# Performance work log

Hardware: AMD Instinct MI355X
Metric: run time of the kernel (lower is better)

The kernel has to match this reference:

```python
import jax, jax.numpy as jnp
import numpy as np

HEADS = 8
LN_EPS = 1e-5

def setup_inputs() -> dict:
    key = jax.random.key(0)
    ks = jax.random.split(key, 12)
    B, T, N, D = 4, 24, 400, 256
    s = 1.0 / np.sqrt(D)
    x = jax.random.normal(ks[0], (B, T, N, D), dtype=jnp.float32)
    adj = jax.random.uniform(ks[1], (B, T, N, N), dtype=jnp.float32)
    Wq = jax.random.uniform(ks[2], (D, D), jnp.float32, -s, s)
    bq = jax.random.uniform(ks[3], (D,), jnp.float32, -s, s)
    Wk = jax.random.uniform(ks[4], (D, D), jnp.float32, -s, s)
    bk = jax.random.uniform(ks[5], (D,), jnp.float32, -s, s)
    Wv = jax.random.uniform(ks[6], (D, D), jnp.float32, -s, s)
    bv = jax.random.uniform(ks[7], (D,), jnp.float32, -s, s)
    gamma = jnp.ones((D,), jnp.float32)
    beta = jnp.zeros((D,), jnp.float32)
    return {"x": x, "adj": adj, "Wq": Wq, "bq": bq, "Wk": Wk, "bk": bk,
            "Wv": Wv, "bv": bv, "gamma": gamma, "beta": beta}

def reference(x, adj, Wq, bq, Wk, bk, Wv, bv, gamma, beta):
    B, T, N, D = x.shape
    H = HEADS
    hd = D // H
    # QKV projections (torch Linear: x @ W.T + b)
    q = (x @ Wq.T + bq).reshape(B, T, N, H, hd)
    k = (x @ Wk.T + bk).reshape(B, T, N, H, hd)
    v = (x @ Wv.T + bv).reshape(B, T, N, H, hd)
    # scores [B,T,H,N,N], scaled then multiplicatively masked by adj
    a = jnp.einsum('btnhd,btmhd->bthnm', q, k) / jnp.sqrt(jnp.float32(hd))
    a = a * adj[:, :, None, :, :]
    a = jax.nn.softmax(a, axis=-1)
    h = jnp.einsum('bthnm,btmhd->btnhd', a, v).reshape(B, T, N, D)
    # dropout is identity in eval; residual + LayerNorm
    y = h + x
    mu = jnp.mean(y, axis=-1, keepdims=True)
    var = jnp.mean((y - mu) ** 2, axis=-1, keepdims=True)
    return (y - mu) * jax.lax.rsqrt(var + LN_EPS) * gamma + beta
```

## Files before the change

### kernel.cpp

```cpp
#include <hip/hip_runtime.h>
#include <cstdint>
#include <cstddef>

typedef unsigned short u16;
typedef __attribute__((ext_vector_type(8))) __bf16 bf16x8;
typedef __attribute__((ext_vector_type(4))) float f32x4;
typedef __attribute__((ext_vector_type(8))) u16 u16x8;
typedef __attribute__((ext_vector_type(4))) u16 u16x4;

#define MTOT   38400
#define DMODEL 256
#define NQKV   768
#define NN     400
#define NBT    96
#define SCALE  0.17677669529663687f

__device__ __forceinline__ u16 f2b(float f){
  __bf16 b = (__bf16)f;
  return __builtin_bit_cast(u16, b);
}

__device__ __forceinline__ void g2l16(const void* g, void* l){
  __builtin_amdgcn_global_load_lds(
      (const __attribute__((address_space(1))) unsigned int*)g,
      (__attribute__((address_space(3))) unsigned int*)l,
      16, 0, 0);
}

__global__ __launch_bounds__(256) void cast_x_kernel(const float* __restrict__ x,
                                                     u16* __restrict__ xb, int n8){
  int i = blockIdx.x * 256 + threadIdx.x;
  if (i >= n8) return;
  const f32x4* xp = (const f32x4*)x;
  f32x4 a = xp[2*i], b = xp[2*i+1];
  u16x8 o;
  o[0]=f2b(a[0]); o[1]=f2b(a[1]); o[2]=f2b(a[2]); o[3]=f2b(a[3]);
  o[4]=f2b(b[0]); o[5]=f2b(b[1]); o[6]=f2b(b[2]); o[7]=f2b(b[3]);
  ((u16x8*)xb)[i] = o;
}

__global__ __launch_bounds__(256) void prep_w_kernel(
    const float* __restrict__ wq, const float* __restrict__ wk, const float* __restrict__ wv,
    const float* __restrict__ bq, const float* __restrict__ bk, const float* __restrict__ bv,
    u16* __restrict__ wqkv, float* __restrict__ bqkv){
  int i = blockIdx.x * 256 + threadIdx.x;
  int g = i >> 14;
  int rem = (i & 16383) * 4;
  const float* w = (g == 0) ? wq : ((g == 1) ? wk : wv);
  float sc = (g == 0) ? SCALE : 1.0f;
  f32x4 v = *(const f32x4*)(w + rem);
  u16x4 o; o[0]=f2b(v[0]*sc); o[1]=f2b(v[1]*sc); o[2]=f2b(v[2]*sc); o[3]=f2b(v[3]*sc);
  *(u16x4*)(wqkv + (size_t)i*4) = o;
  if (i < NQKV) bqkv[i] = (i < 256) ? bq[i]*SCALE : ((i < 512) ? bk[i-256] : bv[i-512]);
}

__global__ __launch_bounds__(256,2) void gemm_qkv_kernel(
    const u16* __restrict__ xb, const u16* __restrict__ wqkv,
    const float* __restrict__ bqkv, u16* __restrict__ qkv){
  __shared__ u16 a_lds[2][128*64];
  __shared__ u16 b_lds[2][128*64];
  const int tid = threadIdx.x, lane = tid & 63, wave = tid >> 6;
  const int bn = blockIdx.x % 6, bm = blockIdx.x / 6;
  const int m0 = bm*128, n0 = bn*128;
  const int wm = (wave>>1)*64, wn = (wave&1)*64;
  const int lr = lane & 15, lk = lane >> 4;
  f32x4 acc[4][4] = {};

  auto stage = [&](int buf, int k0){
    #pragma unroll
    for (int i = 0; i < 4; ++i){
      int off  = (wave*4 + i)*1024 + lane*16;
      int row  = off >> 7;
      int colb = off & 127;
      int scolb = colb ^ ((row & 7) << 4);
      g2l16(xb   + (size_t)(m0+row)*256 + k0 + (scolb>>1), (char*)a_lds[buf] + (wave*4+i)*1024);
      g2l16(wqkv + (size_t)(n0+row)*256 + k0 + (scolb>>1), (char*)b_lds[buf] + (wave*4+i)*1024);
    }
  };

  stage(0, 0);
  #pragma unroll
  for (int ks = 0; ks < 4; ++ks){
    if (ks < 3){
      stage((ks+1)&1, (ks+1)*64);
      asm volatile("s_waitcnt vmcnt(8)" ::: "memory");
    } else {
      asm volatile("s_waitcnt vmcnt(0)" ::: "memory");
    }
    __builtin_amdgcn_s_barrier();
    const char* al = (const char*)a_lds[ks&1];
    const char* bl = (const char*)b_lds[ks&1];
    #pragma unroll
    for (int sub = 0; sub < 2; ++sub){
      bf16x8 af[4], bfr[4];
      #pragma unroll
      for (int i = 0; i < 4; ++i){
        int ra = wm + i*16 + lr;
        af[i]  = *(const bf16x8*)(al + ra*128 + ((sub*64 + lk*16) ^ ((ra&7)<<4)));
        int rb = wn + i*16 + lr;
        bfr[i] = *(const bf16x8*)(bl + rb*128 + ((sub*64 + lk*16) ^ ((rb&7)<<4)));
      }
      #pragma unroll
      for (int i = 0; i < 4; ++i)
        #pragma unroll
        for (int j = 0; j < 4; ++j)
          acc[i][j] = __builtin_amdgcn_mfma_f32_16x16x32_bf16(af[i], bfr[j], acc[i][j], 0, 0, 0);
    }
    __builtin_amdgcn_s_barrier();
  }
  #pragma unroll
  for (int j = 0; j < 4; ++j){
    int n = n0 + wn + j*16 + lr;
    float bias = bqkv[n];
    #pragma unroll
    for (int i = 0; i < 4; ++i){
      int mb = m0 + wm + i*16 + lk*4;
      #pragma unroll
      for (int r = 0; r < 4; ++r)
        qkv[(size_t)(mb + r)*NQKV + n] = f2b(acc[i][j][r] + bias);
    }
  }
}

#define PW_STRIDE 40
#define K_BYTES   25600
#define VT_BYTES  28672
#define ATTN_LDS  (K_BYTES + VT_BYTES + 20480)

__global__ __launch_bounds__(512,4) void attn_kernel(
    const u16* __restrict__ qkv, const float* __restrict__ adj, float* __restrict__ hout){
  extern __shared__ __align__(16) char smem[];
  u16* vT    = (u16*)(smem + K_BYTES);
  u16* p_all = (u16*)(smem + K_BYTES + VT_BYTES);
  const int tid = threadIdx.x, lane = tid & 63, wave = tid >> 6;
  const int h = blockIdx.x / NBT, bt = blockIdx.x % NBT;
  const int lq = lane & 15, lk = lane >> 4;
  const u16* qkvbt = qkv + (size_t)bt*NN*NQKV + h*32;

  {
    const u16* kbase = qkvbt + 256;
    int rsub = lane >> 2;
    int colb = (lane & 3) * 16;
    for (int c = wave; c < 25; c += 8){
      int row  = c*16 + rsub;
      int scol = colb ^ ((row & 3) << 4);
      g2l16(kbase + (size_t)row*NQKV + (scol >> 1), smem + c*1024);
    }
  }
  for (int c = tid; c < 1600; c += 512){
    int row = c >> 2, cc = (c & 3)*8;
    u16x8 v = *(const u16x8*)(qkvbt + 512 + (size_t)row*NQKV + cc);
    #pragma unroll
    for (int e = 0; e < 8; ++e){
      int d = cc + e;
      *(u16*)((char*)vT + d*896 + ((row*2) ^ ((d&7)<<4))) = v[e];
    }
  }
  for (int i = tid; i < 32*48; i += 512){
    int d = i / 48, k = 400 + (i % 48);
    *(u16*)((char*)vT + d*896 + ((k*2) ^ ((d&7)<<4))) = 0;
  }
  __syncthreads();

  const float* adjbt = adj + (size_t)bt*NN*NN;
  u16* pw = p_all + wave*(2*16*PW_STRIDE);
  const f32x4 z = {0.f, 0.f, 0.f, 0.f};

  for (int t25 = wave; t25 < 25; t25 += 8){
    const int q0 = t25*16;
    bf16x8 qf = *(const bf16x8*)(qkvbt + (size_t)(q0 + lq)*NQKV + lk*8);
    const float* arow = adjbt + (size_t)(q0 + lq)*NN;
    f32x4 o0 = z, o1 = z;
    float m_run = -1e30f, l_run = 0.f;
    f32x4 a0 = *(const f32x4*)(arow + lk*4);
    f32x4 a1 = *(const f32x4*)(arow + 16 + lk*4);

    #pragma unroll
    for (int w = 0; w < 12; ++w){
      int r0 = w*32 + lq;
      int r1 = w*32 + 16 + lq;
      bf16x8 k0 = *(const bf16x8*)((const char*)smem + r0*64 + ((lk*16) ^ ((r0 & 3) << 4)));
      bf16x8 k1 = *(const bf16x8*)((const char*)smem + r1*64 + ((lk*16) ^ ((r1 & 3) << 4)));
      __builtin_amdgcn_s_setprio(1);
      f32x4 s0 = __builtin_amdgcn_mfma_f32_16x16x32_bf16(k0, qf, z, 0, 0, 0);
      f32x4 s1 = __builtin_amdgcn_mfma_f32_16x16x32_bf16(k1, qf, z, 0, 0, 0);
      __builtin_amdgcn_s_setprio(0);
      f32x4 ca0 = a0, ca1 = a1;
      if (w < 11){
        a0 = *(const f32x4*)(arow + (w+1)*32 + lk*4);
        a1 = *(const f32x4*)(arow + (w+1)*32 + 16 + lk*4);
      } else {
        a0 = *(const f32x4*)(arow + 384 + lk*4);
      }
      s0 *= ca0; s1 *= ca1;
      float wmx = fmaxf(fmaxf(fmaxf(s0[0],s0[1]), fmaxf(s0[2],s0[3])),
                        fmaxf(fmaxf(s1[0],s1[1]), fmaxf(s1[2],s1[3])));
      wmx = fmaxf(wmx, __shfl_xor(wmx, 16)); wmx = fmaxf(wmx, __shfl_xor(wmx, 32));
      if (!__all(wmx <= m_run + 8.f)){
        float m_new = fmaxf(m_run, wmx);
        float sc = __expf(m_run - m_new);
        m_run = m_new;
        l_run *= sc;
        float osc0 = __shfl(sc, lk*4+0), osc1 = __shfl(sc, lk*4+1);
        float osc2 = __shfl(sc, lk*4+2), osc3 = __shfl(sc, lk*4+3);
        o0[0]*=osc0; o0[1]*=osc1; o0[2]*=osc2; o0[3]*=osc3;
        o1[0]*=osc0; o1[1]*=osc1; o1[2]*=osc2; o1[3]*=osc3;
      }
      f32x4 e0, e1;
      #pragma unroll
      for (int j = 0; j < 4; ++j){ e0[j] = __expf(s0[j] - m_run); e1[j] = __expf(s1[j] - m_run); }
      l_run += (e0[0]+e0[1]+e0[2]+e0[3]) + (e1[0]+e1[1]+e1[2]+e1[3]);
      u16* buf = pw + (w & 1)*(16*PW_STRIDE);
      u16x4 pk0, pk1;
      #pragma unroll
      for (int j = 0; j < 4; ++j){ pk0[j] = f2b(e0[j]); pk1[j] = f2b(e1[j]); }
      *(u16x4*)(buf + lq*PW_STRIDE + lk*4)      = pk0;
      *(u16x4*)(buf + lq*PW_STRIDE + 16 + lk*4) = pk1;
      bf16x8 pf = *(const bf16x8*)((const char*)buf + lq*80 + lk*16);
      int cb = (w*64 + lk*16) ^ ((lq & 7) << 4);
      bf16x8 v0 = *(const bf16x8*)((const char*)vT + lq*896      + cb);
      bf16x8 v1 = *(const bf16x8*)((const char*)vT + (16+lq)*896 + cb);
      o0 = __builtin_amdgcn_mfma_f32_16x16x32_bf16(pf, v0, o0, 0, 0, 0);
      o1 = __builtin_amdgcn_mfma_f32_16x16x32_bf16(pf, v1, o1, 0, 0, 0);
    }
    {
      int r0 = 384 + lq;
      bf16x8 k0 = *(const bf16x8*)((const char*)smem + r0*64 + ((lk*16) ^ ((r0 & 3) << 4)));
      f32x4 s0 = __builtin_amdgcn_mfma_f32_16x16x32_bf16(k0, qf, z, 0, 0, 0);
      s0 *= a0;
      float wmx = fmaxf(fmaxf(s0[0],s0[1]), fmaxf(s0[2],s0[3]));
      wmx = fmaxf(wmx, __shfl_xor(wmx, 16)); wmx = fmaxf(wmx, __shfl_xor(wmx, 32));
      if (!__all(wmx <= m_run + 8.f)){
        float m_new = fmaxf(m_run, wmx);
        float sc = __expf(m_run - m_new);
        m_run = m_new;
        l_run *= sc;
        float osc0 = __shfl(sc, lk*4+0), osc1 = __shfl(sc, lk*4+1);
        float osc2 = __shfl(sc, lk*4+2), osc3 = __shfl(sc, lk*4+3);
        o0[0]*=osc0; o0[1]*=osc1; o0[2]*=osc2; o0[3]*=osc3;
        o1[0]*=osc0; o1[1]*=osc1; o1[2]*=osc2; o1[3]*=osc3;
      }
      f32x4 e0;
      #pragma unroll
      for (int j = 0; j < 4; ++j) e0[j] = __expf(s0[j] - m_run);
      l_run += e0[0]+e0[1]+e0[2]+e0[3];
      u16* buf = pw;
      u16x4 pk0, pk1;
      #pragma unroll
      for (int j = 0; j < 4; ++j){ pk0[j] = f2b(e0[j]); pk1[j] = 0; }
      *(u16x4*)(buf + lq*PW_STRIDE + lk*4)      = pk0;
      *(u16x4*)(buf + lq*PW_STRIDE + 16 + lk*4) = pk1;
      bf16x8 pf = *(const bf16x8*)((const char*)buf + lq*80 + lk*16);
      int cb = (12*64 + lk*16) ^ ((lq & 7) << 4);
      bf16x8 v0 = *(const bf16x8*)((const char*)vT + lq*896      + cb);
      bf16x8 v1 = *(const bf16x8*)((const char*)vT + (16+lq)*896 + cb);
      o0 = __builtin_amdgcn_mfma_f32_16x16x32_bf16(pf, v0, o0, 0, 0, 0);
      o1 = __builtin_amdgcn_mfma_f32_16x16x32_bf16(pf, v1, o1, 0, 0, 0);
    }
    float l = l_run;
    l += __shfl_xor(l, 16); l += __shfl_xor(l, 32);
    float inv = 1.0f / l;
    float* orow = hout + (size_t)(bt*NN + q0)*DMODEL + h*32;
    #pragma unroll
    for (int r = 0; r < 4; ++r){
      float invq = __shfl(inv, lk*4 + r);
      orow[(lk*4 + r)*DMODEL + lq]      = o0[r]*invq;
      orow[(lk*4 + r)*DMODEL + 16 + lq] = o1[r]*invq;
    }
  }
}

__global__ __launch_bounds__(256) void resid_ln_kernel(
    const float* __restrict__ hbuf, const float* __restrict__ x,
    const float* __restrict__ gamma, const float* __restrict__ beta,
    float* __restrict__ out){
  const int wave = threadIdx.x >> 6, lane = threadIdx.x & 63;
  const int row = blockIdx.x*4 + wave;
  const f32x4* hp = (const f32x4*)(hbuf + (size_t)row*DMODEL);
  const f32x4* xp = (const f32x4*)(x    + (size_t)row*DMODEL);
  f32x4 y = hp[lane] + xp[lane];
  float s = y[0] + y[1] + y[2] + y[3];
  s += __shfl_xor(s, 1);  s += __shfl_xor(s, 2);  s += __shfl_xor(s, 4);
  s += __shfl_xor(s, 8);  s += __shfl_xor(s, 16); s += __shfl_xor(s, 32);
  float mu = s * (1.0f/256.0f);
  f32x4 d = y - mu;
  float vs = d[0]*d[0] + d[1]*d[1] + d[2]*d[2] + d[3]*d[3];
  vs += __shfl_xor(vs, 1);  vs += __shfl_xor(vs, 2);  vs += __shfl_xor(vs, 4);
  vs += __shfl_xor(vs, 8);  vs += __shfl_xor(vs, 16); vs += __shfl_xor(vs, 32);
  float rs = rsqrtf(vs * (1.0f/256.0f) + 1e-5f);
  f32x4 g = ((const f32x4*)gamma)[lane];
  f32x4 b = ((const f32x4*)beta)[lane];
  f32x4 o = d*rs*g + b;
  ((f32x4*)(out + (size_t)row*DMODEL))[lane] = o;
}

extern "C" void kernel_launch(void* const* d_in, const int* in_sizes, int n_in,
                              void* d_out, int out_size, void* d_ws, size_t ws_size,
                              hipStream_t stream){
  const float* x     = (const float*)d_in[0];
  const float* adj   = (const float*)d_in[1];
  const float* Wq    = (const float*)d_in[2];
  const float* bq    = (const float*)d_in[3];
  const float* Wk    = (const float*)d_in[4];
  const float* bk    = (const float*)d_in[5];
  const float* Wv    = (const float*)d_in[6];
  const float* bv    = (const float*)d_in[7];
  const float* gamma = (const float*)d_in[8];
  const float* beta  = (const float*)d_in[9];
  float* out = (float*)d_out;
  char* ws = (char*)d_ws;

  u16*   xb   = (u16*)  (ws + 0);
  u16*   wqkv = (u16*)  (ws + 19660800);
  float* bqkv = (float*)(ws + 20054016);
  u16*   qkv  = (u16*)  (ws + 20057088);
  float* hbuf = (float*)(ws + 79039488);

  cast_x_kernel<<<4800, 256, 0, stream>>>(x, xb, 9830400/8);
  prep_w_kernel<<<192, 256, 0, stream>>>(Wq, Wk, Wv, bq, bk, bv, wqkv, bqkv);
  gemm_qkv_kernel<<<1800, 256, 0, stream>>>(xb, wqkv, bqkv, qkv);
  (void)hipFuncSetAttribute((const void*)attn_kernel,
                            hipFuncAttributeMaxDynamicSharedMemorySize, ATTN_LDS);
  attn_kernel<<<768, 512, ATTN_LDS, stream>>>(qkv, adj, hbuf);
  resid_ln_kernel<<<9600, 256, 0, stream>>>(hbuf, x, gamma, beta, out);
}
```

Before: 257.9 us.

## Feed softmax probabilities directly from registers into PV MFMA, drop LDS P buffer

Removes the per-wave LDS staging buffer for the bf16 probability tile. The exp values are packed straight into MFMA A operands, using the upper half zero-padded so the score-MFMA output layout lines up with the PV MFMA. V^T is repacked unswizzled with a 856-byte row stride, and the zero-fill of padding columns is dropped. This saves the LDS store and reload round trip and shrinks LDS use, but issues twice as many PV MFMAs, half of them on zeros, plus duplicated V loads.

```diff
diff --git a/kernel.cpp b/kernel.cpp
--- a/kernel.cpp
+++ b/kernel.cpp
@@ -122,16 +122,14 @@
   }
 }
 
-#define PW_STRIDE 40
 #define K_BYTES   25600
-#define VT_BYTES  28672
-#define ATTN_LDS  (K_BYTES + VT_BYTES + 20480)
+#define VT_BYTES  (32*856)
+#define ATTN_LDS  (K_BYTES + VT_BYTES)
 
 __global__ __launch_bounds__(512,4) void attn_kernel(
     const u16* __restrict__ qkv, const float* __restrict__ adj, float* __restrict__ hout){
   extern __shared__ __align__(16) char smem[];
-  u16* vT    = (u16*)(smem + K_BYTES);
-  u16* p_all = (u16*)(smem + K_BYTES + VT_BYTES);
+  char* vT = smem + K_BYTES;
   const int tid = threadIdx.x, lane = tid & 63, wave = tid >> 6;
   const int h = blockIdx.x / NBT, bt = blockIdx.x % NBT;
   const int lq = lane & 15, lk = lane >> 4;
@@ -151,25 +149,20 @@
     int row = c >> 2, cc = (c & 3)*8;
     u16x8 v = *(const u16x8*)(qkvbt + 512 + (size_t)row*NQKV + cc);
     #pragma unroll
-    for (int e = 0; e < 8; ++e){
-      int d = cc + e;
-      *(u16*)((char*)vT + d*896 + ((row*2) ^ ((d&7)<<4))) = v[e];
-    }
-  }
-  for (int i = tid; i < 32*48; i += 512){
-    int d = i / 48, k = 400 + (i % 48);
-    *(u16*)((char*)vT + d*896 + ((k*2) ^ ((d&7)<<4))) = 0;
+    for (int e = 0; e < 8; ++e)
+      *(u16*)(vT + (cc+e)*856 + row*2) = v[e];
   }
   __syncthreads();
 
   const float* adjbt = adj + (size_t)bt*NN*NN;
-  u16* pw = p_all + wave*(2*16*PW_STRIDE);
   const f32x4 z = {0.f, 0.f, 0.f, 0.f};
 
   for (int t25 = wave; t25 < 25; t25 += 8){
     const int q0 = t25*16;
     bf16x8 qf = *(const bf16x8*)(qkvbt + (size_t)(q0 + lq)*NQKV + lk*8);
     const float* arow = adjbt + (size_t)(q0 + lq)*NN;
+    const char* v0base = vT + lq*856;
+    const char* v1base = vT + (16+lq)*856;
     f32x4 o0 = z, o1 = z;
     float m_run = -1e30f, l_run = 0.f;
     f32x4 a0 = *(const f32x4*)(arow + lk*4);
@@ -206,22 +199,32 @@
         o0[0]*=osc0; o0[1]*=osc1; o0[2]*=osc2; o0[3]*=osc3;
         o1[0]*=osc0; o1[1]*=osc1; o1[2]*=osc2; o1[3]*=osc3;
       }
-      f32x4 e0, e1;
-      #pragma unroll
-      for (int j = 0; j < 4; ++j){ e0[j] = __expf(s0[j] - m_run); e1[j] = __expf(s1[j] - m_run); }
-      l_run += (e0[0]+e0[1]+e0[2]+e0[3]) + (e1[0]+e1[1]+e1[2]+e1[3]);
-      u16* buf = pw + (w & 1)*(16*PW_STRIDE);
-      u16x4 pk0, pk1;
-      #pragma unroll
-      for (int j = 0; j < 4; ++j){ pk0[j] = f2b(e0[j]); pk1[j] = f2b(e1[j]); }
-      *(u16x4*)(buf + lq*PW_STRIDE + lk*4)      = pk0;
-      *(u16x4*)(buf + lq*PW_STRIDE + 16 + lk*4) = pk1;
-      bf16x8 pf = *(const bf16x8*)((const char*)buf + lq*80 + lk*16);
-      int cb = (w*64 + lk*16) ^ ((lq & 7) << 4);
-      bf16x8 v0 = *(const bf16x8*)((const char*)vT + lq*896      + cb);
-      bf16x8 v1 = *(const bf16x8*)((const char*)vT + (16+lq)*896 + cb);
-      o0 = __builtin_amdgcn_mfma_f32_16x16x32_bf16(pf, v0, o0, 0, 0, 0);
-      o1 = __builtin_amdgcn_mfma_f32_16x16x32_bf16(pf, v1, o1, 0, 0, 0);
+      u16x8 A0 = {0,0,0,0,0,0,0,0}, A1 = {0,0,0,0,0,0,0,0};
+      float ls = 0.f;
+      #pragma unroll
+      for (int j = 0; j < 4; ++j){
+        float t0 = __expf(s0[j] - m_run);
+        float t1 = __expf(s1[j] - m_run);
+        A0[j] = f2b(t0); A1[j] = f2b(t1);
+        ls += t0 + t1;
+      }
+      l_run += ls;
+      u16x4 lo00 = *(const u16x4*)(v0base + w*64      + lk*8);
+      u16x4 lo01 = *(const u16x4*)(v0base + w*64 + 32 + lk*8);
+      u16x4 lo10 = *(const u16x4*)(v1base + w*64      + lk*8);
+      u16x4 lo11 = *(const u16x4*)(v1base + w*64 + 32 + lk*8);
+      u16x8 vb00 = {lo00[0],lo00[1],lo00[2],lo00[3], lo00[0],lo00[1],lo00[2],lo00[3]};
+      u16x8 vb01 = {lo01[0],lo01[1],lo01[2],lo01[3], lo01[0],lo01[1],lo01[2],lo01[3]};
+      u16x8 vb10 = {lo10[0],lo10[1],lo10[2],lo10[3], lo10[0],lo10[1],lo10[2],lo10[3]};
+      u16x8 vb11 = {lo11[0],lo11[1],lo11[2],lo11[3], lo11[0],lo11[1],lo11[2],lo11[3]};
+      o0 = __builtin_amdgcn_mfma_f32_16x16x32_bf16(__builtin_bit_cast(bf16x8, A0),
+                                                   __builtin_bit_cast(bf16x8, vb00), o0, 0, 0, 0);
+      o1 = __builtin_amdgcn_mfma_f32_16x16x32_bf16(__builtin_bit_cast(bf16x8, A0),
+                                                   __builtin_bit_cast(bf16x8, vb10), o1, 0, 0, 0);
+      o0 = __builtin_amdgcn_mfma_f32_16x16x32_bf16(__builtin_bit_cast(bf16x8, A1),
+                                                   __builtin_bit_cast(bf16x8, vb01), o0, 0, 0, 0);
+      o1 = __builtin_amdgcn_mfma_f32_16x16x32_bf16(__builtin_bit_cast(bf16x8, A1),
+                                                   __builtin_bit_cast(bf16x8, vb11), o1, 0, 0, 0);
     }
     {
       int r0 = 384 + lq;
@@ -240,22 +243,23 @@
         o0[0]*=osc0; o0[1]*=osc1; o0[2]*=osc2; o0[3]*=osc3;
         o1[0]*=osc0; o1[1]*=osc1; o1[2]*=osc2; o1[3]*=osc3;
       }
-      f32x4 e0;
-      #pragma unroll
-      for (int j = 0; j < 4; ++j) e0[j] = __expf(s0[j] - m_run);
-      l_run += e0[0]+e0[1]+e0[2]+e0[3];
-      u16* buf = pw;
-      u16x4 pk0, pk1;
-      #pragma unroll
-      for (int j = 0; j < 4; ++j){ pk0[j] = f2b(e0[j]); pk1[j] = 0; }
-      *(u16x4*)(buf + lq*PW_STRIDE + lk*4)      = pk0;
-      *(u16x4*)(buf + lq*PW_STRIDE + 16 + lk*4) = pk1;
-      bf16x8 pf = *(const bf16x8*)((const char*)buf + lq*80 + lk*16);
-      int cb = (12*64 + lk*16) ^ ((lq & 7) << 4);
-      bf16x8 v0 = *(const bf16x8*)((const char*)vT + lq*896      + cb);
-      bf16x8 v1 = *(const bf16x8*)((const char*)vT + (16+lq)*896 + cb);
-      o0 = __builtin_amdgcn_mfma_f32_16x16x32_bf16(pf, v0, o0, 0, 0, 0);
-      o1 = __builtin_amdgcn_mfma_f32_16x16x32_bf16(pf, v1, o1, 0, 0, 0);
+      u16x8 A0 = {0,0,0,0,0,0,0,0};
+      float ls = 0.f;
+      #pragma unroll
+      for (int j = 0; j < 4; ++j){
+        float t0 = __expf(s0[j] - m_run);
+        A0[j] = f2b(t0);
+        ls += t0;
+      }
+      l_run += ls;
+      u16x4 lo00 = *(const u16x4*)(v0base + 12*64 + lk*8);
+      u16x4 lo10 = *(const u16x4*)(v1base + 12*64 + lk*8);
+      u16x8 vb00 = {lo00[0],lo00[1],lo00[2],lo00[3], lo00[0],lo00[1],lo00[2],lo00[3]};
+      u16x8 vb10 = {lo10[0],lo10[1],lo10[2],lo10[3], lo10[0],lo10[1],lo10[2],lo10[3]};
+      o0 = __builtin_amdgcn_mfma_f32_16x16x32_bf16(__builtin_bit_cast(bf16x8, A0),
+                                                   __builtin_bit_cast(bf16x8, vb00), o0, 0, 0, 0);
+      o1 = __builtin_amdgcn_mfma_f32_16x16x32_bf16(__builtin_bit_cast(bf16x8, A0),
+                                                   __builtin_bit_cast(bf16x8, vb10), o1, 0, 0, 0);
     }
     float l = l_run;
     l += __shfl_xor(l, 16); l += __shfl_xor(l, 32);
```

After: 254.2 us. Within noise of the previous version (-1.4%).
